# Kernel tuning notes

Measured on AMD Instinct MI355X. Metric: run time of the kernel, lower is better.

The kernel has to match this reference:

```python
import jax, jax.numpy as jnp
import numpy as np

NEG_SLOPE = 0.2  # PyG GATConv default negative_slope


def gat_conv(x, src, dst, W, a_src, a_dst, bias, concat=True):
    """PyG-style GATConv (self-loops already appended to src/dst).
    x: [N, Fin], W: [Fin, H*C], a_src/a_dst: [H, C], bias: [H*C] or [C].
    """
    N = x.shape[0]
    H, C = a_src.shape
    h = (x @ W).reshape(N, H, C)                       # [N, H, C]
    s_src = jnp.einsum('nhc,hc->nh', h, a_src)         # per-node src logit
    s_dst = jnp.einsum('nhc,hc->nh', h, a_dst)         # per-node dst logit
    e = jax.nn.leaky_relu(s_src[src] + s_dst[dst], NEG_SLOPE)   # [E, H]
    # segment softmax over incoming edges of each destination node
    m = jax.ops.segment_max(e, dst, num_segments=N)    # [N, H]
    ex = jnp.exp(e - m[dst])
    denom = jax.ops.segment_sum(ex, dst, num_segments=N)
    alpha = ex / (denom[dst] + 1e-16)                  # [E, H]
    out = jax.ops.segment_sum(h[src] * alpha[:, :, None], dst, num_segments=N)  # [N,H,C]
    out = out.reshape(N, H * C) if concat else out.mean(axis=1)
    return out + bias


def setup_inputs() -> dict:
    key = jax.random.key(0)
    ks = jax.random.split(key, 12)
    N, E = 20000, 320000
    Fin, Hd, Hh = 384, 256, 4
    x = jax.random.normal(ks[0], (N, Fin), dtype=jnp.float32)
    edge_index = jax.random.randint(ks[1], (2, E), 0, N, dtype=jnp.int32)
    s = lambda k, shp, fan: jax.random.normal(k, shp, dtype=jnp.float32) / np.sqrt(fan)
    return {
        'x': x, 'edge_index': edge_index,
        'W1': s(ks[2], (Fin, Hh * Hd), Fin),
        'a_src1': s(ks[3], (Hh, Hd), Hd), 'a_dst1': s(ks[4], (Hh, Hd), Hd),
        'b1': jnp.zeros((Hh * Hd,), jnp.float32),
        'W2': s(ks[5], (Hh * Hd, Hd), Hh * Hd),
        'a_src2': s(ks[6], (1, Hd), Hd), 'a_dst2': s(ks[7], (1, Hd), Hd),
        'b2': jnp.zeros((Hd,), jnp.float32),
        'Wp1': s(ks[8], (Hd, Hd // 2), Hd), 'bp1': jnp.zeros((Hd // 2,), jnp.float32),
        'Wp2': s(ks[9], (Hd // 2, 1), Hd // 2), 'bp2': jnp.zeros((1,), jnp.float32),
    }


def reference(x, edge_index, W1, a_src1, a_dst1, b1, W2, a_src2, a_dst2, b2,
              Wp1, bp1, Wp2, bp2):
    N = x.shape[0]
    loops = jnp.arange(N, dtype=edge_index.dtype)
    src = jnp.concatenate([edge_index[0], loops])  # PyG add_self_loops=True
    dst = jnp.concatenate([edge_index[1], loops])
    h = jax.nn.elu(gat_conv(x, src, dst, W1, a_src1, a_dst1, b1, concat=True))
    h = jax.nn.elu(gat_conv(h, src, dst, W2, a_src2, a_dst2, b2, concat=True))
    graph_features = jnp.mean(h, axis=0, keepdims=True)  # batch=None path
    infl = jax.nn.sigmoid(jax.nn.relu(h @ Wp1 + bp1) @ Wp2 + bp2)
    return h, graph_features, infl
```

## Files before the change

kernel.cpp:

```cpp
#include <hip/hip_runtime.h>

#define NEG_SLOPE 0.2f

typedef __bf16 bf16x8 __attribute__((ext_vector_type(8)));
typedef float floatx4 __attribute__((ext_vector_type(4)));
typedef unsigned short ushortx4 __attribute__((ext_vector_type(4)));
typedef unsigned short ushortx8 __attribute__((ext_vector_type(8)));

__device__ __forceinline__ float eluf(float x) { return x > 0.f ? x : __expf(x) - 1.f; }
__device__ __forceinline__ float lrelu(float x) { return x > 0.f ? x : NEG_SLOPE * x; }

__device__ __forceinline__ unsigned short f2bf(float f) {
    unsigned u = __float_as_uint(f);
    u += 0x7FFFu + ((u >> 16) & 1u);
    return (unsigned short)(u >> 16);
}
__device__ __forceinline__ float bf2f(unsigned short h) {
    return __uint_as_float(((unsigned)h) << 16);
}

__global__ __launch_bounds__(256) void prep_kernel(
        const int* __restrict__ ei, int E, int N, int* __restrict__ counts,
        const float* __restrict__ x, unsigned short* __restrict__ xb,
        const float* __restrict__ W1, unsigned short* __restrict__ w1t,
        const float* __restrict__ W2, unsigned short* __restrict__ w2t,
        const float* __restrict__ Wp1, unsigned short* __restrict__ wp1t,
        const float* __restrict__ as1, const float* __restrict__ ad1, float* __restrict__ U) {
    __shared__ float tile[32][33];
    int b = blockIdx.x;
    int t = threadIdx.x;
    int Et = E + N;
    int nA = (Et + 255) >> 8;
    int nB = (N * 96 + 255) >> 8;
    if (b < nA) {
        int i = b * 256 + t;
        if (i < Et) {
            int d = (i < E) ? ei[E + i] : (i - E);
            atomicAdd(&counts[d], 1);
        }
    } else if (b < nA + nB) {
        int i = (b - nA) * 256 + t;
        if (i < N * 96) {
            float4 v = ((const float4*)x)[i];
            ushortx4 o;
            o[0] = f2bf(v.x); o[1] = f2bf(v.y); o[2] = f2bf(v.z); o[3] = f2bf(v.w);
            *(ushortx4*)(xb + (size_t)i * 4) = o;
        }
    } else if (b < nA + nB + 384) {
        int idx = b - nA - nB;
        int n0 = (idx & 31) * 32, k0 = (idx >> 5) * 32;
        int tx = t & 31, ty = t >> 5;
        #pragma unroll
        for (int i = 0; i < 32; i += 8)
            tile[ty + i][tx] = W1[(size_t)(k0 + ty + i) * 1024 + n0 + tx];
        __syncthreads();
        #pragma unroll
        for (int i = 0; i < 32; i += 8)
            w1t[(size_t)(n0 + ty + i) * 384 + k0 + tx] = f2bf(tile[tx][ty + i]);
    } else if (b < nA + nB + 384 + 256) {
        int idx = b - nA - nB - 384;
        int n0 = (idx & 7) * 32, k0 = (idx >> 3) * 32;
        int tx = t & 31, ty = t >> 5;
        #pragma unroll
        for (int i = 0; i < 32; i += 8)
            tile[ty + i][tx] = W2[(size_t)(k0 + ty + i) * 256 + n0 + tx];
        __syncthreads();
        #pragma unroll
        for (int i = 0; i < 32; i += 8)
            w2t[(size_t)(n0 + ty + i) * 1024 + k0 + tx] = f2bf(tile[tx][ty + i]);
    } else if (b < nA + nB + 384 + 256 + 32) {
        int idx = b - nA - nB - 384 - 256;
        int n0 = (idx & 3) * 32, k0 = (idx >> 2) * 32;
        int tx = t & 31, ty = t >> 5;
        #pragma unroll
        for (int i = 0; i < 32; i += 8)
            tile[ty + i][tx] = Wp1[(size_t)(k0 + ty + i) * 128 + n0 + tx];
        __syncthreads();
        #pragma unroll
        for (int i = 0; i < 32; i += 8)
            wp1t[(size_t)(n0 + ty + i) * 256 + k0 + tx] = f2bf(tile[tx][ty + i]);
    } else {
        int idx = b - nA - nB - 384 - 256 - 32;
        int k = idx * 4 + (t >> 6);
        int lane = t & 63;
        #pragma unroll
        for (int r = 0; r < 8; r++) {
            int h = r & 3;
            const float* a = (r < 4 ? as1 : ad1) + h * 256 + lane * 4;
            const float* w = W1 + (size_t)k * 1024 + h * 256 + lane * 4;
            float4 wv = *(const float4*)w;
            float4 av = *(const float4*)a;
            float p = wv.x * av.x + wv.y * av.y + wv.z * av.z + wv.w * av.w;
            #pragma unroll
            for (int off = 32; off; off >>= 1) p += __shfl_xor(p, off);
            if (lane == 0) U[r * 384 + k] = p;
        }
    }
}

__global__ void scan_kernel(int* __restrict__ counts_cursor, int* __restrict__ row_ptr, int N) {
    __shared__ int s_wsum[16];
    __shared__ int s_carry;
    int t = threadIdx.x;
    int lane = t & 63, wid = t >> 6;
    if (t == 0) { s_carry = 0; row_ptr[0] = 0; }
    __syncthreads();
    for (int start = 0; start < N; start += 1024) {
        int i = start + t;
        int v = (i < N) ? counts_cursor[i] : 0;
        int s = v;
        #pragma unroll
        for (int d = 1; d < 64; d <<= 1) {
            int u = __shfl_up(s, d);
            if (lane >= d) s += u;
        }
        if (lane == 63) s_wsum[wid] = s;
        __syncthreads();
        if (wid == 0) {
            int w = (lane < 16) ? s_wsum[lane] : 0;
            #pragma unroll
            for (int d = 1; d < 16; d <<= 1) {
                int u = __shfl_up(w, d);
                if (lane >= d) w += u;
            }
            if (lane < 16) s_wsum[lane] = w;
        }
        __syncthreads();
        int incl = s + (wid ? s_wsum[wid - 1] : 0) + s_carry;
        if (i < N) { row_ptr[i + 1] = incl; counts_cursor[i] = incl - v; }
        __syncthreads();
        if (t == 0) s_carry += s_wsum[15];
        __syncthreads();
    }
}

__global__ void fill_kernel(const int* __restrict__ ei, int E, int N,
                            int* __restrict__ cursor, int* __restrict__ col) {
    int i = blockIdx.x * blockDim.x + threadIdx.x;
    int Et = E + N;
    if (i >= Et) return;
    int s, d;
    if (i < E) { s = ei[i]; d = ei[E + i]; } else { s = d = i - E; }
    int pos = atomicAdd(&cursor[d], 1);
    col[pos] = s;
}

__global__ void sU_kernel(const unsigned short* __restrict__ xb, const float* __restrict__ U,
                          float* __restrict__ ss1, float* __restrict__ sd1, int N) {
    int wid = (blockIdx.x * blockDim.x + threadIdx.x) >> 6;
    int lane = threadIdx.x & 63;
    if (wid >= N) return;
    int half = lane >> 5, l32 = lane & 31;
    int c0 = l32 * 12;
    const unsigned short* row = xb + (size_t)wid * 384 + c0;
    ushortx8 v8 = *(const ushortx8*)row;
    ushortx4 v4 = *(const ushortx4*)(row + 8);
    float xv[12];
    #pragma unroll
    for (int j = 0; j < 8; j++) xv[j] = bf2f(v8[j]);
    #pragma unroll
    for (int j = 0; j < 4; j++) xv[8 + j] = bf2f(v4[j]);
    float p[4];
    #pragma unroll
    for (int r = 0; r < 4; r++) {
        const float* u = U + (half * 4 + r) * 384 + c0;
        float s = 0.f;
        #pragma unroll
        for (int j = 0; j < 12; j++) s += xv[j] * u[j];
        #pragma unroll
        for (int off = 16; off; off >>= 1) s += __shfl_xor(s, off);
        p[r] = s;
    }
    if (l32 == 0) {
        float* dst = half ? (sd1 + wid * 4) : (ss1 + wid * 4);
        dst[0] = p[0]; dst[1] = p[1]; dst[2] = p[2]; dst[3] = p[3];
    }
}

__global__ void s2_kernel(const unsigned short* __restrict__ h2b, const float* __restrict__ a_src,
                          const float* __restrict__ a_dst, float* __restrict__ ssrc,
                          float* __restrict__ sdst, int N) {
    int wid = (blockIdx.x * blockDim.x + threadIdx.x) >> 6;
    int lane = threadIdx.x & 63;
    if (wid >= N) return;
    ushortx4 v = *(const ushortx4*)(h2b + (size_t)wid * 256 + lane * 4);
    float4 a = ((const float4*)a_src)[lane];
    float4 d = ((const float4*)a_dst)[lane];
    float v0 = bf2f(v[0]), v1 = bf2f(v[1]), v2 = bf2f(v[2]), v3 = bf2f(v[3]);
    float s = v0 * a.x + v1 * a.y + v2 * a.z + v3 * a.w;
    float t = v0 * d.x + v1 * d.y + v2 * d.z + v3 * d.w;
    for (int off = 32; off; off >>= 1) { s += __shfl_xor(s, off); t += __shfl_xor(t, off); }
    if (lane == 0) { ssrc[wid] = s; sdst[wid] = t; }
}

__global__ __launch_bounds__(256) void alpha1_kernel(const float* __restrict__ ssrc,
        const float* __restrict__ sdst, const int* __restrict__ row_ptr,
        const int* __restrict__ col, float* __restrict__ wx, float* __restrict__ den, int N) {
    int wid = (blockIdx.x * blockDim.x + threadIdx.x) >> 6;
    int lane = threadIdx.x & 63;
    if (wid >= N) return;
    int base = row_ptr[wid];
    int deg = row_ptr[wid + 1] - base;
    float sd0 = sdst[wid * 4 + 0], sd1 = sdst[wid * 4 + 1];
    float sd2 = sdst[wid * 4 + 2], sd3 = sdst[wid * 4 + 3];
    float m0 = -1e30f, m1 = -1e30f, m2 = -1e30f, m3 = -1e30f;
    for (int i = lane; i < deg; i += 64) {
        int s = col[base + i];
        const float* sp = ssrc + s * 4;
        m0 = fmaxf(m0, lrelu(sp[0] + sd0));
        m1 = fmaxf(m1, lrelu(sp[1] + sd1));
        m2 = fmaxf(m2, lrelu(sp[2] + sd2));
        m3 = fmaxf(m3, lrelu(sp[3] + sd3));
    }
    #pragma unroll
    for (int off = 32; off; off >>= 1) {
        m0 = fmaxf(m0, __shfl_xor(m0, off));
        m1 = fmaxf(m1, __shfl_xor(m1, off));
        m2 = fmaxf(m2, __shfl_xor(m2, off));
        m3 = fmaxf(m3, __shfl_xor(m3, off));
    }
    float d0 = 0.f, d1 = 0.f, d2 = 0.f, d3 = 0.f;
    for (int i = lane; i < deg; i += 64) {
        int s = col[base + i];
        const float* sp = ssrc + s * 4;
        float4 w4;
        w4.x = __expf(lrelu(sp[0] + sd0) - m0); d0 += w4.x;
        w4.y = __expf(lrelu(sp[1] + sd1) - m1); d1 += w4.y;
        w4.z = __expf(lrelu(sp[2] + sd2) - m2); d2 += w4.z;
        w4.w = __expf(lrelu(sp[3] + sd3) - m3); d3 += w4.w;
        *(float4*)(wx + (size_t)(base + i) * 4) = w4;
    }
    #pragma unroll
    for (int off = 32; off; off >>= 1) {
        d0 += __shfl_xor(d0, off);
        d1 += __shfl_xor(d1, off);
        d2 += __shfl_xor(d2, off);
        d3 += __shfl_xor(d3, off);
    }
    if (lane == 0) {
        den[wid * 4 + 0] = d0; den[wid * 4 + 1] = d1;
        den[wid * 4 + 2] = d2; den[wid * 4 + 3] = d3;
    }
}

__global__ __launch_bounds__(256) void alpha2_kernel(const float* __restrict__ ssrc,
        const float* __restrict__ sdst, const int* __restrict__ row_ptr,
        const int* __restrict__ col, float* __restrict__ wx, float* __restrict__ den, int N) {
    int wid = (blockIdx.x * blockDim.x + threadIdx.x) >> 6;
    int lane = threadIdx.x & 63;
    if (wid >= N) return;
    int base = row_ptr[wid];
    int deg = row_ptr[wid + 1] - base;
    float sd = sdst[wid];
    float m = -1e30f;
    for (int i = lane; i < deg; i += 64) {
        int s = col[base + i];
        m = fmaxf(m, lrelu(ssrc[s] + sd));
    }
    #pragma unroll
    for (int off = 32; off; off >>= 1) m = fmaxf(m, __shfl_xor(m, off));
    float d = 0.f;
    for (int i = lane; i < deg; i += 64) {
        int s = col[base + i];
        float x = __expf(lrelu(ssrc[s] + sd) - m);
        d += x;
        wx[base + i] = x;
    }
    #pragma unroll
    for (int off = 32; off; off >>= 1) d += __shfl_xor(d, off);
    if (lane == 0) den[wid] = d;
}

__global__ __launch_bounds__(256) void aggx_kernel(const unsigned short* __restrict__ xb,
        const float* __restrict__ wx, const float* __restrict__ den,
        const int* __restrict__ row_ptr, const int* __restrict__ col,
        unsigned short* __restrict__ aggxn, int N) {
    __shared__ unsigned short lds[4][1536];
    int t = threadIdx.x;
    int wv = t >> 6;
    int wid = blockIdx.x * 4 + wv;
    int lane = t & 63;
    bool active = wid < N;
    int half = lane >> 5, l32 = lane & 31;
    int c0 = l32 * 12;
    if (active) {
        int base = row_ptr[wid];
        int deg = row_ptr[wid + 1] - base;
        float acc[4][12] = {};
        for (int i = half; i < deg; i += 2) {
            int e = base + i;
            int s = col[e];
            float4 w4 = *(const float4*)(wx + (size_t)e * 4);
            const unsigned short* row = xb + (size_t)s * 384 + c0;
            ushortx8 v8 = *(const ushortx8*)row;
            ushortx4 v4 = *(const ushortx4*)(row + 8);
            float xv[12];
            #pragma unroll
            for (int j = 0; j < 8; j++) xv[j] = bf2f(v8[j]);
            #pragma unroll
            for (int j = 0; j < 4; j++) xv[8 + j] = bf2f(v4[j]);
            #pragma unroll
            for (int j = 0; j < 12; j++) {
                acc[0][j] += w4.x * xv[j];
                acc[1][j] += w4.y * xv[j];
                acc[2][j] += w4.z * xv[j];
                acc[3][j] += w4.w * xv[j];
            }
        }
        #pragma unroll
        for (int h = 0; h < 4; h++)
            #pragma unroll
            for (int j = 0; j < 12; j++)
                acc[h][j] += __shfl_xor(acc[h][j], 32);
        #pragma unroll
        for (int hh = 0; hh < 2; hh++) {
            int h = half * 2 + hh;
            float inv = 1.f / (den[wid * 4 + h] + 1e-16f);
            ushortx8 o8; ushortx4 o4;
            #pragma unroll
            for (int j = 0; j < 8; j++) {
                float v = half ? acc[2 + hh][j] : acc[hh][j];
                o8[j] = f2bf(v * inv);
            }
            #pragma unroll
            for (int j = 0; j < 4; j++) {
                float v = half ? acc[2 + hh][8 + j] : acc[hh][8 + j];
                o4[j] = f2bf(v * inv);
            }
            unsigned short* lp = &lds[wv][h * 384 + c0];
            *(ushortx8*)lp = o8;
            *(ushortx4*)(lp + 8) = o4;
        }
    }
    __syncthreads();
    size_t blockBase = (size_t)blockIdx.x * 4 * 1536;
    const unsigned short* lflat = &lds[0][0];
    #pragma unroll
    for (int j = 0; j < 3; j++) {
        int so = j * 2048 + t * 8;
        int node = blockIdx.x * 4 + so / 1536;
        if (node < N)
            *(ushortx8*)(aggxn + blockBase + so) = *(const ushortx8*)(lflat + so);
    }
}

#define LDK 40

__global__ __launch_bounds__(256) void gemm_l1(const unsigned short* __restrict__ A,
        const unsigned short* __restrict__ Bt, const float* __restrict__ bias,
        unsigned short* __restrict__ Cout, int M) {
    __shared__ unsigned short As[128 * LDK];
    __shared__ unsigned short Bs[128 * LDK];
    int t = threadIdx.x;
    int lane = t & 63, wave = t >> 6;
    int wm = (wave >> 1) * 64, wn = (wave & 1) * 64;
    int q = lane >> 4, l16 = lane & 15;
    int row0 = blockIdx.y * 128, col0 = blockIdx.x * 128;
    int hoff = (col0 >> 8) * 384;
    floatx4 acc[4][4] = {};
    int sg = (t & 7) * 4;
    int sr = t >> 3;
    for (int kt = 0; kt < 384; kt += 32) {
        #pragma unroll
        for (int p = 0; p < 4; p++) {
            int r = sr + p * 32;
            int ga = min(row0 + r, M - 1);
            *(ushortx4*)&As[r * LDK + sg] = *(const ushortx4*)(A + (size_t)ga * 1536 + hoff + kt + sg);
        }
        #pragma unroll
        for (int p = 0; p < 4; p++) {
            int r = sr + p * 32;
            *(ushortx4*)&Bs[r * LDK + sg] = *(const ushortx4*)(Bt + (size_t)(col0 + r) * 384 + kt + sg);
        }
        __syncthreads();
        bf16x8 af[4], bfr[4];
        #pragma unroll
        for (int i = 0; i < 4; i++)
            af[i] = *(const bf16x8*)&As[(wm + i * 16 + l16) * LDK + q * 8];
        #pragma unroll
        for (int j = 0; j < 4; j++)
            bfr[j] = *(const bf16x8*)&Bs[(wn + j * 16 + l16) * LDK + q * 8];
        #pragma unroll
        for (int i = 0; i < 4; i++)
            #pragma unroll
            for (int j = 0; j < 4; j++)
                acc[i][j] = __builtin_amdgcn_mfma_f32_16x16x32_bf16(af[i], bfr[j], acc[i][j], 0, 0, 0);
        __syncthreads();
    }
    float bj[4];
    #pragma unroll
    for (int j = 0; j < 4; j++) bj[j] = bias[col0 + wn + l16 + j * 16];
    #pragma unroll
    for (int i = 0; i < 4; i++) {
        #pragma unroll
        for (int r = 0; r < 4; r++) {
            int grow = row0 + wm + i * 16 + q * 4 + r;
            if (grow < M) {
                unsigned short* cp = Cout + (size_t)grow * 1024 + col0 + wn + l16;
                #pragma unroll
                for (int j = 0; j < 4; j++) cp[j * 16] = f2bf(eluf(acc[i][j][r] + bj[j]));
            }
        }
    }
}

template <int TN>
__global__ __launch_bounds__(256) void gemm_1t(const unsigned short* __restrict__ A,
        const unsigned short* __restrict__ Bt, unsigned short* __restrict__ Cout,
        int M, int N, int K) {
    constexpr int JN = TN / 32;
    __shared__ unsigned short As[128 * LDK];
    __shared__ unsigned short Bs[TN * LDK];
    int t = threadIdx.x;
    int lane = t & 63, wave = t >> 6;
    int wm = (wave >> 1) * 64, wn = (wave & 1) * (TN / 2);
    int q = lane >> 4, l16 = lane & 15;
    int row0 = blockIdx.y * 128, col0 = blockIdx.x * TN;
    floatx4 acc[4][JN] = {};
    int sg = (t & 7) * 4;
    int sr = t >> 3;
    for (int kt = 0; kt < K; kt += 32) {
        #pragma unroll
        for (int p = 0; p < 4; p++) {
            int r = sr + p * 32;
            int ga = min(row0 + r, M - 1);
            *(ushortx4*)&As[r * LDK + sg] = *(const ushortx4*)(A + (size_t)ga * K + kt + sg);
        }
        #pragma unroll
        for (int p = 0; p < TN / 32; p++) {
            int r = sr + p * 32;
            *(ushortx4*)&Bs[r * LDK + sg] = *(const ushortx4*)(Bt + (size_t)(col0 + r) * K + kt + sg);
        }
        __syncthreads();
        bf16x8 af[4], bfr[JN];
        #pragma unroll
        for (int i = 0; i < 4; i++)
            af[i] = *(const bf16x8*)&As[(wm + i * 16 + l16) * LDK + q * 8];
        #pragma unroll
        for (int j = 0; j < JN; j++)
            bfr[j] = *(const bf16x8*)&Bs[(wn + j * 16 + l16) * LDK + q * 8];
        #pragma unroll
        for (int i = 0; i < 4; i++)
            #pragma unroll
            for (int j = 0; j < JN; j++)
                acc[i][j] = __builtin_amdgcn_mfma_f32_16x16x32_bf16(af[i], bfr[j], acc[i][j], 0, 0, 0);
        __syncthreads();
    }
    #pragma unroll
    for (int i = 0; i < 4; i++) {
        #pragma unroll
        for (int r = 0; r < 4; r++) {
            int grow = row0 + wm + i * 16 + q * 4 + r;
            if (grow < M) {
                unsigned short* cp = Cout + (size_t)grow * N + col0 + wn + l16;
                #pragma unroll
                for (int j = 0; j < JN; j++) cp[j * 16] = f2bf(acc[i][j][r]);
            }
        }
    }
}

__global__ __launch_bounds__(256) void agg2_kernel(const unsigned short* __restrict__ h2b,
        const float* __restrict__ wx, const float* __restrict__ den,
        const int* __restrict__ row_ptr, const int* __restrict__ col,
        const float* __restrict__ bias, float* __restrict__ out,
        unsigned short* __restrict__ outb, int N) {
    int wid = (blockIdx.x * blockDim.x + threadIdx.x) >> 6;
    int lane = threadIdx.x & 63;
    if (wid >= N) return;
    int base = row_ptr[wid];
    int deg = row_ptr[wid + 1] - base;
    float4 a = {0, 0, 0, 0};
    int c = lane * 4;
    int i = 0;
    for (; i + 1 < deg; i += 2) {
        int s0 = col[base + i], s1 = col[base + i + 1];
        float x0 = wx[base + i], x1 = wx[base + i + 1];
        ushortx4 v0 = *(const ushortx4*)(h2b + (size_t)s0 * 256 + c);
        ushortx4 v1 = *(const ushortx4*)(h2b + (size_t)s1 * 256 + c);
        a.x += x0 * bf2f(v0[0]) + x1 * bf2f(v1[0]);
        a.y += x0 * bf2f(v0[1]) + x1 * bf2f(v1[1]);
        a.z += x0 * bf2f(v0[2]) + x1 * bf2f(v1[2]);
        a.w += x0 * bf2f(v0[3]) + x1 * bf2f(v1[3]);
    }
    if (i < deg) {
        int s0 = col[base + i];
        float x0 = wx[base + i];
        ushortx4 v0 = *(const ushortx4*)(h2b + (size_t)s0 * 256 + c);
        a.x += x0 * bf2f(v0[0]); a.y += x0 * bf2f(v0[1]);
        a.z += x0 * bf2f(v0[2]); a.w += x0 * bf2f(v0[3]);
    }
    float inv = 1.f / (den[wid] + 1e-16f);
    float4 o;
    o.x = eluf(a.x * inv + bias[c + 0]);
    o.y = eluf(a.y * inv + bias[c + 1]);
    o.z = eluf(a.z * inv + bias[c + 2]);
    o.w = eluf(a.w * inv + bias[c + 3]);
    *(float4*)(out + (size_t)wid * 256 + c) = o;
    ushortx4 ob;
    ob[0] = f2bf(o.x); ob[1] = f2bf(o.y); ob[2] = f2bf(o.z); ob[3] = f2bf(o.w);
    *(ushortx4*)(outb + (size_t)wid * 256 + c) = ob;
}

__global__ __launch_bounds__(256) void tail_kernel(const float* __restrict__ h,
        const unsigned short* __restrict__ hbf, const unsigned short* __restrict__ wp1t,
        const float* __restrict__ bp1, const float* __restrict__ Wp2,
        const float* __restrict__ bp2, float* __restrict__ gf, float* __restrict__ infl, int M) {
    int b = blockIdx.x;
    int nInfl = (M + 127) / 128;
    if (b < nInfl) {
        __shared__ unsigned short As[128 * LDK];
        __shared__ unsigned short Bs[128 * LDK];
        __shared__ float partial[2][128];
        int t = threadIdx.x;
        int lane = t & 63, wave = t >> 6;
        int wm = (wave >> 1) * 64, wn = (wave & 1) * 64;
        int q = lane >> 4, l16 = lane & 15;
        int row0 = b * 128;
        floatx4 acc[4][4] = {};
        int sg = (t & 7) * 4;
        int sr = t >> 3;
        for (int kt = 0; kt < 256; kt += 32) {
            #pragma unroll
            for (int p = 0; p < 4; p++) {
                int r = sr + p * 32;
                int ga = min(row0 + r, M - 1);
                *(ushortx4*)&As[r * LDK + sg] = *(const ushortx4*)(hbf + (size_t)ga * 256 + kt + sg);
                *(ushortx4*)&Bs[r * LDK + sg] = *(const ushortx4*)(wp1t + (size_t)r * 256 + kt + sg);
            }
            __syncthreads();
            bf16x8 af[4], bfr[4];
            #pragma unroll
            for (int i = 0; i < 4; i++)
                af[i] = *(const bf16x8*)&As[(wm + i * 16 + l16) * LDK + q * 8];
            #pragma unroll
            for (int j = 0; j < 4; j++)
                bfr[j] = *(const bf16x8*)&Bs[(wn + j * 16 + l16) * LDK + q * 8];
            #pragma unroll
            for (int i = 0; i < 4; i++)
                #pragma unroll
                for (int j = 0; j < 4; j++)
                    acc[i][j] = __builtin_amdgcn_mfma_f32_16x16x32_bf16(af[i], bfr[j], acc[i][j], 0, 0, 0);
            __syncthreads();
        }
        float b1v[4], w2v[4];
        #pragma unroll
        for (int j = 0; j < 4; j++) {
            int colj = wn + j * 16 + l16;
            b1v[j] = bp1[colj];
            w2v[j] = Wp2[colj];
        }
        #pragma unroll
        for (int i = 0; i < 4; i++) {
            #pragma unroll
            for (int r = 0; r < 4; r++) {
                float s = fmaxf(acc[i][0][r] + b1v[0], 0.f) * w2v[0]
                        + fmaxf(acc[i][1][r] + b1v[1], 0.f) * w2v[1]
                        + fmaxf(acc[i][2][r] + b1v[2], 0.f) * w2v[2]
                        + fmaxf(acc[i][3][r] + b1v[3], 0.f) * w2v[3];
                #pragma unroll
                for (int off = 1; off < 16; off <<= 1) s += __shfl_xor(s, off);
                if (l16 == 0) partial[wave & 1][wm + i * 16 + q * 4 + r] = s;
            }
        }
        __syncthreads();
        if (t < 128) {
            int row = row0 + t;
            if (row < M) {
                float v = partial[0][t] + partial[1][t] + bp2[0];
                infl[row] = 1.f / (1.f + __expf(-v));
            }
        }
    } else {
        int bb = b - nInfl;
        int c = threadIdx.x;
        int per = (M + 159) / 160;
        int n0 = bb * per;
        int n1 = min(M, n0 + per);
        float a0 = 0.f, a1 = 0.f, a2 = 0.f, a3 = 0.f;
        float a4 = 0.f, a5 = 0.f, a6 = 0.f, a7 = 0.f;
        int n = n0;
        for (; n + 8 <= n1; n += 8) {
            a0 += h[(size_t)(n + 0) * 256 + c];
            a1 += h[(size_t)(n + 1) * 256 + c];
            a2 += h[(size_t)(n + 2) * 256 + c];
            a3 += h[(size_t)(n + 3) * 256 + c];
            a4 += h[(size_t)(n + 4) * 256 + c];
            a5 += h[(size_t)(n + 5) * 256 + c];
            a6 += h[(size_t)(n + 6) * 256 + c];
            a7 += h[(size_t)(n + 7) * 256 + c];
        }
        for (; n < n1; n++) a0 += h[(size_t)n * 256 + c];
        float acc = ((a0 + a1) + (a2 + a3)) + ((a4 + a5) + (a6 + a7));
        atomicAdd(&gf[c], acc * (1.0f / M));
    }
}

extern "C" void kernel_launch(void* const* d_in, const int* in_sizes, int n_in,
                              void* d_out, int out_size, void* d_ws, size_t ws_size,
                              hipStream_t stream) {
    const float* x   = (const float*)d_in[0];
    const int*   ei  = (const int*)d_in[1];
    const float* W1  = (const float*)d_in[2];
    const float* as1 = (const float*)d_in[3];
    const float* ad1 = (const float*)d_in[4];
    const float* b1  = (const float*)d_in[5];
    const float* W2  = (const float*)d_in[6];
    const float* as2 = (const float*)d_in[7];
    const float* ad2 = (const float*)d_in[8];
    const float* b2  = (const float*)d_in[9];
    const float* Wp1 = (const float*)d_in[10];
    const float* bp1 = (const float*)d_in[11];
    const float* Wp2 = (const float*)d_in[12];
    const float* bp2 = (const float*)d_in[13];

    const int N  = in_sizes[0] / 384;
    const int E  = in_sizes[1] / 2;
    const int Et = E + N;

    char* wsp = (char*)d_ws;
    unsigned short* xb    = (unsigned short*)wsp; wsp += (size_t)N * 384  * sizeof(short);
    unsigned short* aggxn = (unsigned short*)wsp; wsp += (size_t)N * 1536 * sizeof(short);
    unsigned short* h1eb  = (unsigned short*)wsp; wsp += (size_t)N * 1024 * sizeof(short);
    unsigned short* h2b   = (unsigned short*)wsp; wsp += (size_t)N * 256  * sizeof(short);
    unsigned short* hbf   = (unsigned short*)wsp; wsp += (size_t)N * 256  * sizeof(short);
    unsigned short* w1t   = (unsigned short*)wsp; wsp += (size_t)1024 * 384 * sizeof(short);
    unsigned short* w2t   = (unsigned short*)wsp; wsp += (size_t)256 * 1024 * sizeof(short);
    unsigned short* wp1t  = (unsigned short*)wsp; wsp += (size_t)128 * 256 * sizeof(short);
    float* U   = (float*)wsp; wsp += (size_t)8 * 384 * sizeof(float);
    float* ss1 = (float*)wsp; wsp += (size_t)N * 4 * sizeof(float);
    float* sd1 = (float*)wsp; wsp += (size_t)N * 4 * sizeof(float);
    float* ss2 = (float*)wsp; wsp += (size_t)N * sizeof(float);
    float* sd2 = (float*)wsp; wsp += (size_t)N * sizeof(float);
    float* den1 = (float*)wsp; wsp += (size_t)N * 4 * sizeof(float);
    float* den2 = (float*)wsp; wsp += (size_t)N * sizeof(float);
    float* wx1  = (float*)wsp; wsp += (size_t)Et * 4 * sizeof(float);
    float* wx2  = (float*)wsp; wsp += (size_t)Et * sizeof(float);
    int* row_ptr = (int*)wsp; wsp += (size_t)(N + 1) * sizeof(int);
    int* cursor  = (int*)wsp; wsp += (size_t)N * sizeof(int);
    int* col     = (int*)wsp;

    float* out_h  = (float*)d_out;
    float* out_gf = out_h + (size_t)N * 256;
    float* out_if = out_gf + 256;

    hipMemsetAsync(cursor, 0, (size_t)N * sizeof(int), stream);
    int nA = (Et + 255) / 256;
    int nB = (N * 96 + 255) / 256;
    int nPrep = nA + nB + 384 + 256 + 32 + 96;
    prep_kernel<<<nPrep, 256, 0, stream>>>(ei, E, N, cursor, x, xb, W1, w1t, W2, w2t, Wp1, wp1t, as1, ad1, U);
    scan_kernel<<<1, 1024, 0, stream>>>(cursor, row_ptr, N);
    fill_kernel<<<nA, 256, 0, stream>>>(ei, E, N, cursor, col);

    sU_kernel<<<(N + 3) / 4, 256, 0, stream>>>(xb, U, ss1, sd1, N);
    alpha1_kernel<<<(N + 3) / 4, 256, 0, stream>>>(ss1, sd1, row_ptr, col, wx1, den1, N);
    aggx_kernel<<<(N + 3) / 4, 256, 0, stream>>>(xb, wx1, den1, row_ptr, col, aggxn, N);
    gemm_l1<<<dim3(8, (N + 127) / 128), 256, 0, stream>>>(aggxn, w1t, b1, h1eb, N);

    gemm_1t<64><<<dim3(4, (N + 127) / 128), 256, 0, stream>>>(h1eb, w2t, h2b, N, 256, 1024);
    s2_kernel<<<(N + 3) / 4, 256, 0, stream>>>(h2b, as2, ad2, ss2, sd2, N);
    alpha2_kernel<<<(N + 3) / 4, 256, 0, stream>>>(ss2, sd2, row_ptr, col, wx2, den2, N);
    agg2_kernel<<<(N + 3) / 4, 256, 0, stream>>>(h2b, wx2, den2, row_ptr, col, b2, out_h, hbf, N);

    hipMemsetAsync(out_gf, 0, 256 * sizeof(float), stream);
    tail_kernel<<<(N + 127) / 128 + 160, 256, 0, stream>>>(out_h, hbf, wp1t, bp1, Wp2, bp2, out_gf, out_if, N);
}
```

Measured before the change: 375.9 us.

## Double-buffer GEMM tiles with async global-to-LDS loads

Both layer GEMMs now stage A and B tiles straight from global memory into LDS with the global_load_lds builtin, using two buffers so the next K-slice loads while the current one feeds MFMA. The padded LDK stride is dropped to a packed stride of 32, and the layer-2 GEMM is specialized with fixed dimensions. The aim is to hide global-load latency and remove the register round-trip for staging. The packed layout may add LDS bank conflicts, and there is no explicit wait on the async loads before the barrier, so correctness depends on how the compiler handles the vmcnt wait.

After: 357.8 us. 4.8% less time.

```diff
diff --git a/kernel.cpp b/kernel.cpp
--- a/kernel.cpp
+++ b/kernel.cpp
@@ -17,6 +17,13 @@
 }
 __device__ __forceinline__ float bf2f(unsigned short h) {
     return __uint_as_float(((unsigned)h) << 16);
+}
+
+__device__ __forceinline__ void async16(const unsigned short* g, unsigned short* l) {
+    __builtin_amdgcn_global_load_lds(
+        (const __attribute__((address_space(1))) unsigned int*)g,
+        (__attribute__((address_space(3))) unsigned int*)l,
+        16, 0, 0);
 }
 
 __global__ __launch_bounds__(256) void prep_kernel(
@@ -349,8 +356,8 @@
 __global__ __launch_bounds__(256) void gemm_l1(const unsigned short* __restrict__ A,
         const unsigned short* __restrict__ Bt, const float* __restrict__ bias,
         unsigned short* __restrict__ Cout, int M) {
-    __shared__ unsigned short As[128 * LDK];
-    __shared__ unsigned short Bs[128 * LDK];
+    __shared__ unsigned short As[2][128 * 32];
+    __shared__ unsigned short Bs[2][128 * 32];
     int t = threadIdx.x;
     int lane = t & 63, wave = t >> 6;
     int wm = (wave >> 1) * 64, wn = (wave & 1) * 64;
@@ -358,28 +365,30 @@
     int row0 = blockIdx.y * 128, col0 = blockIdx.x * 128;
     int hoff = (col0 >> 8) * 384;
     floatx4 acc[4][4] = {};
-    int sg = (t & 7) * 4;
-    int sr = t >> 3;
-    for (int kt = 0; kt < 384; kt += 32) {
-        #pragma unroll
-        for (int p = 0; p < 4; p++) {
-            int r = sr + p * 32;
-            int ga = min(row0 + r, M - 1);
-            *(ushortx4*)&As[r * LDK + sg] = *(const ushortx4*)(A + (size_t)ga * 1536 + hoff + kt + sg);
-        }
-        #pragma unroll
-        for (int p = 0; p < 4; p++) {
-            int r = sr + p * 32;
-            *(ushortx4*)&Bs[r * LDK + sg] = *(const ushortx4*)(Bt + (size_t)(col0 + r) * 384 + kt + sg);
-        }
-        __syncthreads();
+    int srow = t >> 2, skc = (t & 3) * 8;
+    const unsigned short* Ag0 = A + (size_t)min(row0 + srow, M - 1) * 1536 + hoff + skc;
+    const unsigned short* Ag1 = A + (size_t)min(row0 + srow + 64, M - 1) * 1536 + hoff + skc;
+    const unsigned short* Bg0 = Bt + (size_t)(col0 + srow) * 384 + skc;
+    const unsigned short* Bg1 = Bt + (size_t)(col0 + srow + 64) * 384 + skc;
+#define STG_L1(buf, kt) \
+    async16(Ag0 + (kt), &As[buf][t * 8]); \
+    async16(Ag1 + (kt), &As[buf][2048 + t * 8]); \
+    async16(Bg0 + (kt), &Bs[buf][t * 8]); \
+    async16(Bg1 + (kt), &Bs[buf][2048 + t * 8]);
+    STG_L1(0, 0)
+    __syncthreads();
+    #pragma unroll
+    for (int ti = 0; ti < 12; ++ti) {
+        int cur = ti & 1;
+        if (ti < 11) { STG_L1(cur ^ 1, (ti + 1) * 32) }
+        __builtin_amdgcn_sched_barrier(0);
         bf16x8 af[4], bfr[4];
         #pragma unroll
         for (int i = 0; i < 4; i++)
-            af[i] = *(const bf16x8*)&As[(wm + i * 16 + l16) * LDK + q * 8];
+            af[i] = *(const bf16x8*)&As[cur][(wm + i * 16 + l16) * 32 + q * 8];
         #pragma unroll
         for (int j = 0; j < 4; j++)
-            bfr[j] = *(const bf16x8*)&Bs[(wn + j * 16 + l16) * LDK + q * 8];
+            bfr[j] = *(const bf16x8*)&Bs[cur][(wn + j * 16 + l16) * 32 + q * 8];
         #pragma unroll
         for (int i = 0; i < 4; i++)
             #pragma unroll
@@ -387,6 +396,7 @@
                 acc[i][j] = __builtin_amdgcn_mfma_f32_16x16x32_bf16(af[i], bfr[j], acc[i][j], 0, 0, 0);
         __syncthreads();
     }
+#undef STG_L1
     float bj[4];
     #pragma unroll
     for (int j = 0; j < 4; j++) bj[j] = bias[col0 + wn + l16 + j * 16];
@@ -404,57 +414,55 @@
     }
 }
 
-template <int TN>
-__global__ __launch_bounds__(256) void gemm_1t(const unsigned short* __restrict__ A,
-        const unsigned short* __restrict__ Bt, unsigned short* __restrict__ Cout,
-        int M, int N, int K) {
-    constexpr int JN = TN / 32;
-    __shared__ unsigned short As[128 * LDK];
-    __shared__ unsigned short Bs[TN * LDK];
+__global__ __launch_bounds__(256) void gemm_l2(const unsigned short* __restrict__ A,
+        const unsigned short* __restrict__ Bt, unsigned short* __restrict__ Cout, int M) {
+    __shared__ unsigned short As[2][128 * 32];
+    __shared__ unsigned short Bs[2][64 * 32];
     int t = threadIdx.x;
     int lane = t & 63, wave = t >> 6;
-    int wm = (wave >> 1) * 64, wn = (wave & 1) * (TN / 2);
+    int wm = (wave >> 1) * 64, wn = (wave & 1) * 32;
     int q = lane >> 4, l16 = lane & 15;
-    int row0 = blockIdx.y * 128, col0 = blockIdx.x * TN;
-    floatx4 acc[4][JN] = {};
-    int sg = (t & 7) * 4;
-    int sr = t >> 3;
-    for (int kt = 0; kt < K; kt += 32) {
-        #pragma unroll
-        for (int p = 0; p < 4; p++) {
-            int r = sr + p * 32;
-            int ga = min(row0 + r, M - 1);
-            *(ushortx4*)&As[r * LDK + sg] = *(const ushortx4*)(A + (size_t)ga * K + kt + sg);
-        }
-        #pragma unroll
-        for (int p = 0; p < TN / 32; p++) {
-            int r = sr + p * 32;
-            *(ushortx4*)&Bs[r * LDK + sg] = *(const ushortx4*)(Bt + (size_t)(col0 + r) * K + kt + sg);
-        }
-        __syncthreads();
-        bf16x8 af[4], bfr[JN];
+    int row0 = blockIdx.y * 128, col0 = blockIdx.x * 64;
+    floatx4 acc[4][2] = {};
+    int srow = t >> 2, skc = (t & 3) * 8;
+    const unsigned short* Ag0 = A + (size_t)min(row0 + srow, M - 1) * 1024 + skc;
+    const unsigned short* Ag1 = A + (size_t)min(row0 + srow + 64, M - 1) * 1024 + skc;
+    const unsigned short* Bg0 = Bt + (size_t)(col0 + srow) * 1024 + skc;
+#define STG_L2(buf, kt) \
+    async16(Ag0 + (kt), &As[buf][t * 8]); \
+    async16(Ag1 + (kt), &As[buf][2048 + t * 8]); \
+    async16(Bg0 + (kt), &Bs[buf][t * 8]);
+    STG_L2(0, 0)
+    __syncthreads();
+    #pragma unroll
+    for (int ti = 0; ti < 32; ++ti) {
+        int cur = ti & 1;
+        if (ti < 31) { STG_L2(cur ^ 1, (ti + 1) * 32) }
+        __builtin_amdgcn_sched_barrier(0);
+        bf16x8 af[4], bfr[2];
         #pragma unroll
         for (int i = 0; i < 4; i++)
-            af[i] = *(const bf16x8*)&As[(wm + i * 16 + l16) * LDK + q * 8];
-        #pragma unroll
-        for (int j = 0; j < JN; j++)
-            bfr[j] = *(const bf16x8*)&Bs[(wn + j * 16 + l16) * LDK + q * 8];
+            af[i] = *(const bf16x8*)&As[cur][(wm + i * 16 + l16) * 32 + q * 8];
+        #pragma unroll
+        for (int j = 0; j < 2; j++)
+            bfr[j] = *(const bf16x8*)&Bs[cur][(wn + j * 16 + l16) * 32 + q * 8];
         #pragma unroll
         for (int i = 0; i < 4; i++)
             #pragma unroll
-            for (int j = 0; j < JN; j++)
+            for (int j = 0; j < 2; j++)
                 acc[i][j] = __builtin_amdgcn_mfma_f32_16x16x32_bf16(af[i], bfr[j], acc[i][j], 0, 0, 0);
         __syncthreads();
     }
+#undef STG_L2
     #pragma unroll
     for (int i = 0; i < 4; i++) {
         #pragma unroll
         for (int r = 0; r < 4; r++) {
             int grow = row0 + wm + i * 16 + q * 4 + r;
             if (grow < M) {
-                unsigned short* cp = Cout + (size_t)grow * N + col0 + wn + l16;
+                unsigned short* cp = Cout + (size_t)grow * 256 + col0 + wn + l16;
                 #pragma unroll
-                for (int j = 0; j < JN; j++) cp[j * 16] = f2bf(acc[i][j][r]);
+                for (int j = 0; j < 2; j++) cp[j * 16] = f2bf(acc[i][j][r]);
             }
         }
     }
@@ -657,7 +665,7 @@
     aggx_kernel<<<(N + 3) / 4, 256, 0, stream>>>(xb, wx1, den1, row_ptr, col, aggxn, N);
     gemm_l1<<<dim3(8, (N + 127) / 128), 256, 0, stream>>>(aggxn, w1t, b1, h1eb, N);
 
-    gemm_1t<64><<<dim3(4, (N + 127) / 128), 256, 0, stream>>>(h1eb, w2t, h2b, N, 256, 1024);
+    gemm_l2<<<dim3(4, (N + 127) / 128), 256, 0, stream>>>(h1eb, w2t, h2b, N);
     s2_kernel<<<(N + 3) / 4, 256, 0, stream>>>(h2b, as2, ad2, ss2, sd2, N);
     alpha2_kernel<<<(N + 3) / 4, 256, 0, stream>>>(ss2, sd2, row_ptr, col, wx2, den2, N);
     agg2_kernel<<<(N + 3) / 4, 256, 0, stream>>>(h2b, wx2, den2, row_ptr, col, b2, out_h, hbf, N);
```
